# Kernel optimization log

Hardware: AMD Instinct MI355X
Metric: run time of the kernel (lower is better)

## Reference

```python
import jax, jax.numpy as jnp
import numpy as np

U = 100000   # num_users
I = 50000    # num_items
N = U + I    # total nodes
D = 64       # embed_size
L = 3        # n_layers
E = 2000000  # num edges
EPS = 1e-12  # F.normalize default eps


def setup_inputs() -> dict:
    key = jax.random.key(0)
    k1, k2, k3, k4 = jax.random.split(key, 4)
    user_emb = jax.random.normal(k1, (U, D), dtype=jnp.float32) * 0.1
    item_emb = jax.random.normal(k2, (I, D), dtype=jnp.float32) * 0.1
    rows = jax.random.randint(k3, (E,), 0, N, dtype=jnp.int32)
    cols = jax.random.randint(k4, (E,), 0, N, dtype=jnp.int32)
    return {"user_emb": user_emb, "item_emb": item_emb, "rows": rows, "cols": cols}


def _spmm(vals, rows, cols, x):
    # sparse [N,N] @ dense [N,D] via gather + segment reduce
    return jax.ops.segment_sum(vals[:, None] * x[cols], rows, num_segments=N)


def _l2norm(x):
    return x / jnp.maximum(jnp.linalg.norm(x, axis=1, keepdims=True), EPS)


def reference(user_emb, item_emb, rows, cols):
    emb0 = jnp.concatenate([user_emb, item_emb], axis=0)  # [N, D]

    # laplacian_adj: G = D^-1/2 A D^-1/2 on the same edge set
    deg = jax.ops.segment_sum(jnp.ones((E,), emb0.dtype), rows, num_segments=N)
    d_is = jnp.where(deg > 0, deg ** -0.5, 0.0)
    g_vals = d_is[rows] * d_is[cols]  # [E]

    cur = emb0
    acc = emb0
    user_fine, item_fine = [], []
    for _ in range(L):
        gnn = _spmm(g_vals, rows, cols, cur)  # [N, D]
        # fine_laplacian_adj: cosine-sim edge scores, row-normalized
        gr = _l2norm(gnn[rows])
        gc = _l2norm(gnn[cols])
        scores = (jnp.sum(gr * gc, axis=1) + 1.0) * 0.5  # [E] in [0,1]
        rowsum = jax.ops.segment_sum(scores, rows, num_segments=N)
        d_inv = jnp.where(rowsum > 0, 1.0 / rowsum, 0.0)
        fine = _spmm(d_inv[rows] * scores, rows, cols, cur)  # [N, D]
        cur = gnn + fine
        acc = acc + cur
        user_fine.append(fine[:U])
        item_fine.append(fine[U:])

    u_embs = acc[:U]
    i_embs = acc[U:]
    return (u_embs, i_embs, jnp.stack(user_fine, 0), jnp.stack(item_fine, 0))
```

## Files before the change

kernel.cpp:

```cpp
#include <hip/hip_runtime.h>

namespace {

typedef unsigned short u16;
typedef __attribute__((__ext_vector_type__(2))) float f32x2;
typedef __attribute__((__ext_vector_type__(4))) float f32x4;

constexpr int Un = 100000;
constexpr int In = 50000;
constexpr int Nn = 150000;
constexpr int D  = 64;
constexpr int Ln = 3;
constexpr int En = 2000000;
constexpr int CHUNK = 1024;
constexpr int NB = (Nn + CHUNK - 1) / CHUNK;

__device__ __forceinline__ u16 f2bf(float f) {
    unsigned u = __float_as_uint(f);
    unsigned r = (u + 0x7FFFu + ((u >> 16) & 1u)) >> 16;
    return (u16)r;
}
__device__ __forceinline__ float bflo(unsigned u) {
    return __uint_as_float(u << 16);
}
__device__ __forceinline__ float bfhi(unsigned u) {
    return __uint_as_float(u & 0xFFFF0000u);
}
__device__ __forceinline__ unsigned pack2(float lo, float hi) {
    return (unsigned)f2bf(lo) | ((unsigned)f2bf(hi) << 16);
}

__device__ __forceinline__ f32x2 pkfma(f32x2 a, f32x2 b, f32x2 c) {
    f32x2 d;
    asm("v_pk_fma_f32 %0, %1, %2, %3" : "=v"(d) : "v"(a), "v"(b), "v"(c));
    return d;
}
__device__ __forceinline__ f32x2 pkadd(f32x2 a, f32x2 b) {
    f32x2 d;
    asm("v_pk_add_f32 %0, %1, %2" : "=v"(d) : "v"(a), "v"(b));
    return d;
}

__device__ __forceinline__ float dpp_add8(float x) {
    x += __uint_as_float((unsigned)__builtin_amdgcn_update_dpp(
        0, (int)__float_as_uint(x), 0xB1, 0xF, 0xF, true));
    x += __uint_as_float((unsigned)__builtin_amdgcn_update_dpp(
        0, (int)__float_as_uint(x), 0x4E, 0xF, 0xF, true));
    x += __uint_as_float((unsigned)__builtin_amdgcn_update_dpp(
        0, (int)__float_as_uint(x), 0x141, 0xF, 0xF, true));
    return x;
}

__device__ __forceinline__ void unp8(uint4 q, f32x2* o) {
    o[0].x = bflo(q.x); o[0].y = bfhi(q.x);
    o[1].x = bflo(q.y); o[1].y = bfhi(q.y);
    o[2].x = bflo(q.z); o[2].y = bfhi(q.z);
    o[3].x = bflo(q.w); o[3].y = bfhi(q.w);
}

__global__ void count_kernel(const int* __restrict__ rows, int* __restrict__ deg,
                             int* __restrict__ eoff) {
    int e = blockIdx.x * blockDim.x + threadIdx.x;
    if (e < En) eoff[e] = atomicAdd(&deg[rows[e]], 1);
}

__global__ void scan_partial(const int* __restrict__ deg, float* __restrict__ d_is,
                             int* __restrict__ bsum) {
    int tid = threadIdx.x;
    int base = blockIdx.x * CHUNK + tid * 4;
    int s = 0;
#pragma unroll
    for (int i = 0; i < 4; ++i) {
        int idx = base + i;
        if (idx < Nn) {
            int d = deg[idx];
            s += d;
            d_is[idx] = d > 0 ? rsqrtf((float)d) : 0.f;
        }
    }
    __shared__ int sh[256];
    sh[tid] = s;
    __syncthreads();
    for (int o = 128; o > 0; o >>= 1) {
        if (tid < o) sh[tid] += sh[tid + o];
        __syncthreads();
    }
    if (tid == 0) bsum[blockIdx.x] = sh[0];
}

__global__ void scan_top(int* __restrict__ bsum, int* __restrict__ row_ptr) {
    __shared__ int sh[256];
    int tid = threadIdx.x;
    int v = (tid < NB) ? bsum[tid] : 0;
    sh[tid] = v;
    __syncthreads();
    for (int o = 1; o < 256; o <<= 1) {
        int t = (tid >= o) ? sh[tid - o] : 0;
        __syncthreads();
        sh[tid] += t;
        __syncthreads();
    }
    if (tid < NB) bsum[tid] = sh[tid] - v;
    if (tid == 255) row_ptr[Nn] = sh[255];
}

__global__ void scan_final(const int* __restrict__ deg, const int* __restrict__ bsum,
                           int* __restrict__ row_ptr) {
    int tid = threadIdx.x;
    int base = blockIdx.x * CHUNK + tid * 4;
    int v[4];
    int ts = 0;
#pragma unroll
    for (int i = 0; i < 4; ++i) {
        int idx = base + i;
        v[i] = (idx < Nn) ? deg[idx] : 0;
        ts += v[i];
    }
    __shared__ int sh[256];
    sh[tid] = ts;
    __syncthreads();
    for (int o = 1; o < 256; o <<= 1) {
        int t = (tid >= o) ? sh[tid - o] : 0;
        __syncthreads();
        sh[tid] += t;
        __syncthreads();
    }
    int excl = bsum[blockIdx.x] + sh[tid] - ts;
#pragma unroll
    for (int i = 0; i < 4; ++i) {
        int idx = base + i;
        if (idx < Nn) row_ptr[idx] = excl;
        excl += v[i];
    }
}

__global__ void fill_kernel(const int* __restrict__ rows, const int* __restrict__ cols,
                            const int* __restrict__ row_ptr, const int* __restrict__ eoff,
                            int* __restrict__ col_off) {
    int e = blockIdx.x * blockDim.x + threadIdx.x;
    if (e >= En) return;
    col_off[row_ptr[rows[e]] + eoff[e]] = cols[e] << 7;
}

__global__ void init_kernel(const float* __restrict__ ue, const float* __restrict__ ie,
                            const float* __restrict__ d_is,
                            float* __restrict__ out, u16* __restrict__ cur,
                            u16* __restrict__ S) {
    int i = (blockIdx.x * 256 + threadIdx.x) * 4;
    if (i >= Nn * D) return;
    const float* src = (i < Un * D) ? (ue + i) : (ie + (i - Un * D));
    float4 v = *(const float4*)src;
    *(float4*)(out + i) = v;
    ushort4 q;
    q.x = f2bf(v.x); q.y = f2bf(v.y); q.z = f2bf(v.z); q.w = f2bf(v.w);
    *(ushort4*)(cur + i) = q;
    float ds = d_is[i >> 6];
    ushort4 qs;
    qs.x = f2bf(v.x * ds); qs.y = f2bf(v.y * ds);
    qs.z = f2bf(v.z * ds); qs.w = f2bf(v.w * ds);
    *(ushort4*)(S + i) = qs;
}

__global__ __launch_bounds__(256) void spmm_gnn(const u16* __restrict__ S_,
                                                u16* __restrict__ Qn_,
                                                const int* __restrict__ row_ptr,
                                                const int* __restrict__ col_off,
                                                const float* __restrict__ d_is,
                                                float* __restrict__ normv) {
    int r = (blockIdx.x * 256 + threadIdx.x) >> 6;
    if (r >= Nn) return;
    int lane = threadIdx.x & 63;
    int g = lane >> 3, l = lane & 7;
    unsigned l16 = (unsigned)l * 16u;
    const char* pS = (const char*)S_;
    int s = row_ptr[r], t = row_ptr[r + 1];
    float dr = d_is[r];
    f32x2 z; z.x = 0.f; z.y = 0.f;
    f32x2 a2[4] = {z, z, z, z};
    int deg = t - s;
    int nfull = deg >> 3;
    int rem = deg & 7;
    int jb = s + g;
#pragma unroll 2
    for (int i = 0; i < nfull; ++i) {
        unsigned off = (unsigned)col_off[jb + i * 8];
        uint4 q = *(const uint4*)(pS + (off + l16));
        f32x2 x2[4];
        unp8(q, x2);
#pragma unroll
        for (int p = 0; p < 4; ++p) a2[p] = pkadd(a2[p], x2[p]);
    }
    if (g < rem) {
        unsigned off = (unsigned)col_off[jb + nfull * 8];
        uint4 q = *(const uint4*)(pS + (off + l16));
        f32x2 x2[4];
        unp8(q, x2);
#pragma unroll
        for (int p = 0; p < 4; ++p) a2[p] = pkadd(a2[p], x2[p]);
    }
    float a[8] = {a2[0].x, a2[0].y, a2[1].x, a2[1].y,
                  a2[2].x, a2[2].y, a2[3].x, a2[3].y};
#pragma unroll
    for (int k = 0; k < 8; ++k) {
        a[k] += __shfl_xor(a[k], 8);
        a[k] += __shfl_xor(a[k], 16);
        a[k] += __shfl_xor(a[k], 32);
    }
    float sq = 0.f;
#pragma unroll
    for (int k = 0; k < 8; ++k) sq = fmaf(a[k], a[k], sq);
    sq = dpp_add8(sq);
    if (g == 0) {
        float gn = dr * sqrtf(sq);
        float nrm = fmaxf(gn, 1e-12f);
        float scale = dr / nrm;
        normv[r] = nrm;
        unsigned ro = ((unsigned)r << 7) + l16;
        uint4 on;
        on.x = pack2(a[0] * scale, a[1] * scale);
        on.y = pack2(a[2] * scale, a[3] * scale);
        on.z = pack2(a[4] * scale, a[5] * scale);
        on.w = pack2(a[6] * scale, a[7] * scale);
        *(uint4*)((char*)Qn_ + ro) = on;
    }
}

__global__ __launch_bounds__(256) void score_fine_kernel(const u16* __restrict__ A_,
                                                         const u16* __restrict__ Qn_,
                                                         u16* __restrict__ C_,
                                                         u16* __restrict__ S_,
                                                         const float* __restrict__ normv,
                                                         const float* __restrict__ d_is,
                                                         const int* __restrict__ row_ptr,
                                                         const int* __restrict__ col_off,
                                                         float* __restrict__ out, int layer) {
    int r = (blockIdx.x * 256 + threadIdx.x) >> 6;
    if (r >= Nn) return;
    int lane = threadIdx.x & 63;
    int g = lane >> 3, l = lane & 7;
    unsigned l16 = (unsigned)l * 16u;
    const char* pQn = (const char*)Qn_;
    const char* pA  = (const char*)A_;
    int s = row_ptr[r], t = row_ptr[r + 1];
    unsigned ro = ((unsigned)r << 7) + l16;
    uint4 qbn = *(const uint4*)(pQn + ro);
    float nrm = normv[r];
    float dsr = d_is[r];
    f32x2 b2[4];
    unp8(qbn, b2);
    f32x2 z; z.x = 0.f; z.y = 0.f;
    f32x2 facc[4] = {z, z, z, z};
    float rowsum = 0.f;
    int deg = t - s;
    int nfull = deg >> 3;
    int rem = deg & 7;
    int jb = s + g;
#pragma unroll 2
    for (int i = 0; i < nfull; ++i) {
        unsigned off = (unsigned)col_off[jb + i * 8];
        unsigned vo = off + l16;
        uint4 qx = *(const uint4*)(pQn + vo);
        uint4 qy = *(const uint4*)(pA + vo);
        f32x2 x2[4];
        unp8(qx, x2);
        f32x2 d2 = pkfma(b2[0], x2[0], z);
        d2 = pkfma(b2[1], x2[1], d2);
        d2 = pkfma(b2[2], x2[2], d2);
        d2 = pkfma(b2[3], x2[3], d2);
        float d = dpp_add8(d2.x + d2.y);
        float sc = fmaf(d, 0.5f, 0.5f);
        rowsum += sc;
        f32x2 y2[4];
        unp8(qy, y2);
        f32x2 sc2; sc2.x = sc; sc2.y = sc;
#pragma unroll
        for (int p = 0; p < 4; ++p) facc[p] = pkfma(sc2, y2[p], facc[p]);
    }
    if (g < rem) {
        unsigned off = (unsigned)col_off[jb + nfull * 8];
        unsigned vo = off + l16;
        uint4 qx = *(const uint4*)(pQn + vo);
        uint4 qy = *(const uint4*)(pA + vo);
        f32x2 x2[4];
        unp8(qx, x2);
        f32x2 d2 = pkfma(b2[0], x2[0], z);
        d2 = pkfma(b2[1], x2[1], d2);
        d2 = pkfma(b2[2], x2[2], d2);
        d2 = pkfma(b2[3], x2[3], d2);
        float d = dpp_add8(d2.x + d2.y);
        float sc = fmaf(d, 0.5f, 0.5f);
        rowsum += sc;
        f32x2 y2[4];
        unp8(qy, y2);
        f32x2 sc2; sc2.x = sc; sc2.y = sc;
#pragma unroll
        for (int p = 0; p < 4; ++p) facc[p] = pkfma(sc2, y2[p], facc[p]);
    }
    float f[8] = {facc[0].x, facc[0].y, facc[1].x, facc[1].y,
                  facc[2].x, facc[2].y, facc[3].x, facc[3].y};
    rowsum += __shfl_xor(rowsum, 8);
    rowsum += __shfl_xor(rowsum, 16);
    rowsum += __shfl_xor(rowsum, 32);
#pragma unroll
    for (int k = 0; k < 8; ++k) {
        f[k] += __shfl_xor(f[k], 8);
        f[k] += __shfl_xor(f[k], 16);
        f[k] += __shfl_xor(f[k], 32);
    }
    float di = rowsum > 0.f ? 1.f / rowsum : 0.f;
#pragma unroll
    for (int k = 0; k < 8; ++k) f[k] *= di;
    if (g == 0) {
        float bb[8] = {b2[0].x, b2[0].y, b2[1].x, b2[1].y,
                       b2[2].x, b2[2].y, b2[3].x, b2[3].y};
        float cn[8];
#pragma unroll
        for (int k = 0; k < 8; ++k) cn[k] = fmaf(bb[k], nrm, f[k]);
        uint4 qn;
        qn.x = pack2(cn[0], cn[1]); qn.y = pack2(cn[2], cn[3]);
        qn.z = pack2(cn[4], cn[5]); qn.w = pack2(cn[6], cn[7]);
        *(uint4*)((char*)C_ + ro) = qn;
        if (layer != Ln - 1) {
            uint4 qs;
            qs.x = pack2(cn[0] * dsr, cn[1] * dsr);
            qs.y = pack2(cn[2] * dsr, cn[3] * dsr);
            qs.z = pack2(cn[4] * dsr, cn[5] * dsr);
            qs.w = pack2(cn[6] * dsr, cn[7] * dsr);
            *(uint4*)((char*)S_ + ro) = qs;
        }
        float* op = out + (size_t)r * D + l * 8;
        float4 a0 = ((float4*)op)[0], a1 = ((float4*)op)[1];
        a0.x += cn[0]; a0.y += cn[1]; a0.z += cn[2]; a0.w += cn[3];
        a1.x += cn[4]; a1.y += cn[5]; a1.z += cn[6]; a1.w += cn[7];
        ((float4*)op)[0] = a0;
        ((float4*)op)[1] = a1;
        size_t fo;
        if (r < Un)
            fo = (size_t)Nn * D + (size_t)layer * Un * D + (size_t)r * D + l * 8;
        else
            fo = (size_t)Nn * D + (size_t)Ln * Un * D + (size_t)layer * In * D
                 + (size_t)(r - Un) * D + l * 8;
        f32x4 f0, f1;
        f0.x = f[0]; f0.y = f[1]; f0.z = f[2]; f0.w = f[3];
        f1.x = f[4]; f1.y = f[5]; f1.z = f[6]; f1.w = f[7];
        __builtin_nontemporal_store(f0, (f32x4*)(out + fo));
        __builtin_nontemporal_store(f1, (f32x4*)(out + fo) + 1);
    }
}

}

extern "C" void kernel_launch(void* const* d_in, const int* in_sizes, int n_in,
                              void* d_out, int out_size, void* d_ws, size_t ws_size,
                              hipStream_t stream) {
    const float* user_emb = (const float*)d_in[0];
    const float* item_emb = (const float*)d_in[1];
    const int* rows = (const int*)d_in[2];
    const int* cols = (const int*)d_in[3];
    float* out = (float*)d_out;

    char* ws = (char*)d_ws;
    size_t off = 0;
    auto alloc = [&](size_t bytes) -> void* {
        void* p = ws + off;
        off += (bytes + 255) & ~size_t(255);
        return p;
    };
    u16*   buf0    = (u16*)  alloc((size_t)Nn * D * 2);
    u16*   buf1    = (u16*)  alloc((size_t)Nn * D * 2);
    u16*   buf2    = (u16*)  alloc((size_t)Nn * D * 2);
    u16*   buf3    = (u16*)  alloc((size_t)Nn * D * 2);
    int*   col_off = (int*)  alloc((size_t)(En + 8) * 4);
    int*   deg     = (int*)  alloc((size_t)Nn * 4);
    int*   row_ptr = (int*)  alloc((size_t)(Nn + 1) * 4);
    float* d_is    = (float*)alloc((size_t)Nn * 4);
    float* normv   = (float*)alloc((size_t)Nn * 4);
    int*   bsum    = (int*)  alloc(4096);
    int*   eoff    = (int*)buf2;
    (void)ws_size; (void)in_sizes; (void)n_in; (void)out_size;

    hipMemsetAsync(deg, 0, (size_t)Nn * 4, stream);

    const int EB = (En + 255) / 256;
    count_kernel<<<EB, 256, 0, stream>>>(rows, deg, eoff);
    scan_partial<<<NB, 256, 0, stream>>>(deg, d_is, bsum);
    scan_top<<<1, 256, 0, stream>>>(bsum, row_ptr);
    scan_final<<<NB, 256, 0, stream>>>(deg, bsum, row_ptr);
    fill_kernel<<<EB, 256, 0, stream>>>(rows, cols, row_ptr, eoff, col_off);
    init_kernel<<<(Nn * D / 4 + 255) / 256, 256, 0, stream>>>(user_emb, item_emb, d_is,
                                                              out, buf0, buf3);

    const int RB = Nn / 4;
    u16* P = buf0;
    u16* R = buf1;
    u16* Qn = buf2;
    u16* S  = buf3;
    for (int l = 0; l < Ln; ++l) {
        spmm_gnn<<<RB, 256, 0, stream>>>(S, Qn, row_ptr, col_off, d_is, normv);
        score_fine_kernel<<<RB, 256, 0, stream>>>(P, Qn, R, S, normv, d_is,
                                                  row_ptr, col_off, out, l);
        u16* tmp = P; P = R; R = tmp;
    }
}
```

Measured before the change: 788.2 us.

## Map one row per 8-lane group with degree-sorted row ordering

```diff
diff --git a/kernel.cpp b/kernel.cpp
--- a/kernel.cpp
+++ b/kernel.cpp
@@ -14,6 +14,8 @@
 constexpr int En = 2000000;
 constexpr int CHUNK = 1024;
 constexpr int NB = (Nn + CHUNK - 1) / CHUNK;
+constexpr int DCAP = 128;
+constexpr int NW = Nn / 8;
 
 __device__ __forceinline__ u16 f2bf(float f) {
     unsigned u = __float_as_uint(f);
@@ -140,6 +142,49 @@
     int e = blockIdx.x * blockDim.x + threadIdx.x;
     if (e >= En) return;
     col_off[row_ptr[rows[e]] + eoff[e]] = cols[e] << 7;
+}
+
+__global__ void hist_kernel(const int* __restrict__ deg, int* __restrict__ hist) {
+    __shared__ int lh[DCAP];
+    int tid = threadIdx.x;
+    if (tid < DCAP) lh[tid] = 0;
+    __syncthreads();
+    int i = blockIdx.x * 256 + tid;
+    if (i < Nn) atomicAdd(&lh[min(deg[i], DCAP - 1)], 1);
+    __syncthreads();
+    if (tid < DCAP) {
+        int v = lh[tid];
+        if (v) atomicAdd(&hist[tid], v);
+    }
+}
+
+__global__ void hist_scan(int* __restrict__ hist) {
+    __shared__ int sh[DCAP];
+    int tid = threadIdx.x;
+    int v = hist[tid];
+    sh[tid] = v;
+    __syncthreads();
+    for (int o = 1; o < DCAP; o <<= 1) {
+        int t = (tid >= o) ? sh[tid - o] : 0;
+        __syncthreads();
+        sh[tid] += t;
+        __syncthreads();
+    }
+    hist[tid] = sh[tid] - v;
+}
+
+__global__ void perm_kernel(const int* __restrict__ deg, const int* __restrict__ row_ptr,
+                            const float* __restrict__ d_is, int* __restrict__ hist,
+                            int4* __restrict__ srt) {
+    int i = blockIdx.x * 256 + threadIdx.x;
+    if (i >= Nn) return;
+    int p = atomicAdd(&hist[min(deg[i], DCAP - 1)], 1);
+    int4 v;
+    v.x = row_ptr[i];
+    v.y = row_ptr[i + 1];
+    v.z = __float_as_int(d_is[i]);
+    v.w = i;
+    srt[p] = v;
 }
 
 __global__ void init_kernel(const float* __restrict__ ue, const float* __restrict__ ie,
@@ -163,101 +208,82 @@
 
 __global__ __launch_bounds__(256) void spmm_gnn(const u16* __restrict__ S_,
                                                 u16* __restrict__ Qn_,
-                                                const int* __restrict__ row_ptr,
+                                                const int4* __restrict__ srt,
                                                 const int* __restrict__ col_off,
-                                                const float* __restrict__ d_is,
-                                                float* __restrict__ normv) {
-    int r = (blockIdx.x * 256 + threadIdx.x) >> 6;
-    if (r >= Nn) return;
+                                                float* __restrict__ normv_s) {
+    int w = (blockIdx.x * 256 + threadIdx.x) >> 6;
+    if (w >= NW) return;
     int lane = threadIdx.x & 63;
     int g = lane >> 3, l = lane & 7;
     unsigned l16 = (unsigned)l * 16u;
+    int wb = w * 8 + g;
+    int4 q4 = srt[wb];
+    int s = q4.x, t = q4.y;
+    float dr = __int_as_float(q4.z);
+    int r = q4.w;
     const char* pS = (const char*)S_;
-    int s = row_ptr[r], t = row_ptr[r + 1];
-    float dr = d_is[r];
     f32x2 z; z.x = 0.f; z.y = 0.f;
     f32x2 a2[4] = {z, z, z, z};
-    int deg = t - s;
-    int nfull = deg >> 3;
-    int rem = deg & 7;
-    int jb = s + g;
 #pragma unroll 2
-    for (int i = 0; i < nfull; ++i) {
-        unsigned off = (unsigned)col_off[jb + i * 8];
+    for (int j = s; j < t; ++j) {
+        unsigned off = (unsigned)col_off[j];
         uint4 q = *(const uint4*)(pS + (off + l16));
         f32x2 x2[4];
         unp8(q, x2);
 #pragma unroll
         for (int p = 0; p < 4; ++p) a2[p] = pkadd(a2[p], x2[p]);
     }
-    if (g < rem) {
-        unsigned off = (unsigned)col_off[jb + nfull * 8];
-        uint4 q = *(const uint4*)(pS + (off + l16));
-        f32x2 x2[4];
-        unp8(q, x2);
-#pragma unroll
-        for (int p = 0; p < 4; ++p) a2[p] = pkadd(a2[p], x2[p]);
-    }
-    float a[8] = {a2[0].x, a2[0].y, a2[1].x, a2[1].y,
-                  a2[2].x, a2[2].y, a2[3].x, a2[3].y};
-#pragma unroll
-    for (int k = 0; k < 8; ++k) {
-        a[k] += __shfl_xor(a[k], 8);
-        a[k] += __shfl_xor(a[k], 16);
-        a[k] += __shfl_xor(a[k], 32);
-    }
     float sq = 0.f;
 #pragma unroll
-    for (int k = 0; k < 8; ++k) sq = fmaf(a[k], a[k], sq);
+    for (int p = 0; p < 4; ++p) {
+        sq = fmaf(a2[p].x, a2[p].x, sq);
+        sq = fmaf(a2[p].y, a2[p].y, sq);
+    }
     sq = dpp_add8(sq);
-    if (g == 0) {
-        float gn = dr * sqrtf(sq);
-        float nrm = fmaxf(gn, 1e-12f);
-        float scale = dr / nrm;
-        normv[r] = nrm;
-        unsigned ro = ((unsigned)r << 7) + l16;
-        uint4 on;
-        on.x = pack2(a[0] * scale, a[1] * scale);
-        on.y = pack2(a[2] * scale, a[3] * scale);
-        on.z = pack2(a[4] * scale, a[5] * scale);
-        on.w = pack2(a[6] * scale, a[7] * scale);
-        *(uint4*)((char*)Qn_ + ro) = on;
-    }
+    float gn = dr * sqrtf(sq);
+    float nrm = fmaxf(gn, 1e-12f);
+    float scale = dr / nrm;
+    if (l == 0) normv_s[wb] = nrm;
+    unsigned ro = ((unsigned)r << 7) + l16;
+    uint4 on;
+    on.x = pack2(a2[0].x * scale, a2[0].y * scale);
+    on.y = pack2(a2[1].x * scale, a2[1].y * scale);
+    on.z = pack2(a2[2].x * scale, a2[2].y * scale);
+    on.w = pack2(a2[3].x * scale, a2[3].y * scale);
+    *(uint4*)((char*)Qn_ + ro) = on;
 }
 
 __global__ __launch_bounds__(256) void score_fine_kernel(const u16* __restrict__ A_,
                                                          const u16* __restrict__ Qn_,
                                                          u16* __restrict__ C_,
                                                          u16* __restrict__ S_,
-                                                         const float* __restrict__ normv,
-                                                         const float* __restrict__ d_is,
-                                                         const int* __restrict__ row_ptr,
+                                                         const float* __restrict__ normv_s,
+                                                         const int4* __restrict__ srt,
                                                          const int* __restrict__ col_off,
                                                          float* __restrict__ out, int layer) {
-    int r = (blockIdx.x * 256 + threadIdx.x) >> 6;
-    if (r >= Nn) return;
+    int w = (blockIdx.x * 256 + threadIdx.x) >> 6;
+    if (w >= NW) return;
     int lane = threadIdx.x & 63;
     int g = lane >> 3, l = lane & 7;
     unsigned l16 = (unsigned)l * 16u;
+    int wb = w * 8 + g;
+    int4 q4 = srt[wb];
+    int s = q4.x, t = q4.y;
+    float dsr = __int_as_float(q4.z);
+    int r = q4.w;
+    float nrm = normv_s[wb];
     const char* pQn = (const char*)Qn_;
     const char* pA  = (const char*)A_;
-    int s = row_ptr[r], t = row_ptr[r + 1];
     unsigned ro = ((unsigned)r << 7) + l16;
     uint4 qbn = *(const uint4*)(pQn + ro);
-    float nrm = normv[r];
-    float dsr = d_is[r];
     f32x2 b2[4];
     unp8(qbn, b2);
     f32x2 z; z.x = 0.f; z.y = 0.f;
     f32x2 facc[4] = {z, z, z, z};
     float rowsum = 0.f;
-    int deg = t - s;
-    int nfull = deg >> 3;
-    int rem = deg & 7;
-    int jb = s + g;
 #pragma unroll 2
-    for (int i = 0; i < nfull; ++i) {
-        unsigned off = (unsigned)col_off[jb + i * 8];
+    for (int j = s; j < t; ++j) {
+        unsigned off = (unsigned)col_off[j];
         unsigned vo = off + l16;
         uint4 qx = *(const uint4*)(pQn + vo);
         uint4 qy = *(const uint4*)(pA + vo);
@@ -276,76 +302,43 @@
 #pragma unroll
         for (int p = 0; p < 4; ++p) facc[p] = pkfma(sc2, y2[p], facc[p]);
     }
-    if (g < rem) {
-        unsigned off = (unsigned)col_off[jb + nfull * 8];
-        unsigned vo = off + l16;
-        uint4 qx = *(const uint4*)(pQn + vo);
-        uint4 qy = *(const uint4*)(pA + vo);
-        f32x2 x2[4];
-        unp8(qx, x2);
-        f32x2 d2 = pkfma(b2[0], x2[0], z);
-        d2 = pkfma(b2[1], x2[1], d2);
-        d2 = pkfma(b2[2], x2[2], d2);
-        d2 = pkfma(b2[3], x2[3], d2);
-        float d = dpp_add8(d2.x + d2.y);
-        float sc = fmaf(d, 0.5f, 0.5f);
-        rowsum += sc;
-        f32x2 y2[4];
-        unp8(qy, y2);
-        f32x2 sc2; sc2.x = sc; sc2.y = sc;
-#pragma unroll
-        for (int p = 0; p < 4; ++p) facc[p] = pkfma(sc2, y2[p], facc[p]);
-    }
-    float f[8] = {facc[0].x, facc[0].y, facc[1].x, facc[1].y,
-                  facc[2].x, facc[2].y, facc[3].x, facc[3].y};
-    rowsum += __shfl_xor(rowsum, 8);
-    rowsum += __shfl_xor(rowsum, 16);
-    rowsum += __shfl_xor(rowsum, 32);
-#pragma unroll
-    for (int k = 0; k < 8; ++k) {
-        f[k] += __shfl_xor(f[k], 8);
-        f[k] += __shfl_xor(f[k], 16);
-        f[k] += __shfl_xor(f[k], 32);
-    }
     float di = rowsum > 0.f ? 1.f / rowsum : 0.f;
-#pragma unroll
-    for (int k = 0; k < 8; ++k) f[k] *= di;
-    if (g == 0) {
-        float bb[8] = {b2[0].x, b2[0].y, b2[1].x, b2[1].y,
-                       b2[2].x, b2[2].y, b2[3].x, b2[3].y};
-        float cn[8];
-#pragma unroll
-        for (int k = 0; k < 8; ++k) cn[k] = fmaf(bb[k], nrm, f[k]);
-        uint4 qn;
-        qn.x = pack2(cn[0], cn[1]); qn.y = pack2(cn[2], cn[3]);
-        qn.z = pack2(cn[4], cn[5]); qn.w = pack2(cn[6], cn[7]);
-        *(uint4*)((char*)C_ + ro) = qn;
-        if (layer != Ln - 1) {
-            uint4 qs;
-            qs.x = pack2(cn[0] * dsr, cn[1] * dsr);
-            qs.y = pack2(cn[2] * dsr, cn[3] * dsr);
-            qs.z = pack2(cn[4] * dsr, cn[5] * dsr);
-            qs.w = pack2(cn[6] * dsr, cn[7] * dsr);
-            *(uint4*)((char*)S_ + ro) = qs;
-        }
-        float* op = out + (size_t)r * D + l * 8;
-        float4 a0 = ((float4*)op)[0], a1 = ((float4*)op)[1];
-        a0.x += cn[0]; a0.y += cn[1]; a0.z += cn[2]; a0.w += cn[3];
-        a1.x += cn[4]; a1.y += cn[5]; a1.z += cn[6]; a1.w += cn[7];
-        ((float4*)op)[0] = a0;
-        ((float4*)op)[1] = a1;
-        size_t fo;
-        if (r < Un)
-            fo = (size_t)Nn * D + (size_t)layer * Un * D + (size_t)r * D + l * 8;
-        else
-            fo = (size_t)Nn * D + (size_t)Ln * Un * D + (size_t)layer * In * D
-                 + (size_t)(r - Un) * D + l * 8;
-        f32x4 f0, f1;
-        f0.x = f[0]; f0.y = f[1]; f0.z = f[2]; f0.w = f[3];
-        f1.x = f[4]; f1.y = f[5]; f1.z = f[6]; f1.w = f[7];
-        __builtin_nontemporal_store(f0, (f32x4*)(out + fo));
-        __builtin_nontemporal_store(f1, (f32x4*)(out + fo) + 1);
-    }
+    float f[8] = {facc[0].x * di, facc[0].y * di, facc[1].x * di, facc[1].y * di,
+                  facc[2].x * di, facc[2].y * di, facc[3].x * di, facc[3].y * di};
+    float bb[8] = {b2[0].x, b2[0].y, b2[1].x, b2[1].y,
+                   b2[2].x, b2[2].y, b2[3].x, b2[3].y};
+    float cn[8];
+#pragma unroll
+    for (int k = 0; k < 8; ++k) cn[k] = fmaf(bb[k], nrm, f[k]);
+    uint4 qn;
+    qn.x = pack2(cn[0], cn[1]); qn.y = pack2(cn[2], cn[3]);
+    qn.z = pack2(cn[4], cn[5]); qn.w = pack2(cn[6], cn[7]);
+    *(uint4*)((char*)C_ + ro) = qn;
+    if (layer != Ln - 1) {
+        uint4 qs;
+        qs.x = pack2(cn[0] * dsr, cn[1] * dsr);
+        qs.y = pack2(cn[2] * dsr, cn[3] * dsr);
+        qs.z = pack2(cn[4] * dsr, cn[5] * dsr);
+        qs.w = pack2(cn[6] * dsr, cn[7] * dsr);
+        *(uint4*)((char*)S_ + ro) = qs;
+    }
+    float* op = out + (size_t)r * D + l * 8;
+    float4 a0 = ((float4*)op)[0], a1 = ((float4*)op)[1];
+    a0.x += cn[0]; a0.y += cn[1]; a0.z += cn[2]; a0.w += cn[3];
+    a1.x += cn[4]; a1.y += cn[5]; a1.z += cn[6]; a1.w += cn[7];
+    ((float4*)op)[0] = a0;
+    ((float4*)op)[1] = a1;
+    size_t fo;
+    if (r < Un)
+        fo = (size_t)Nn * D + (size_t)layer * Un * D + (size_t)r * D + l * 8;
+    else
+        fo = (size_t)Nn * D + (size_t)Ln * Un * D + (size_t)layer * In * D
+             + (size_t)(r - Un) * D + l * 8;
+    f32x4 f0, f1;
+    f0.x = f[0]; f0.y = f[1]; f0.z = f[2]; f0.w = f[3];
+    f1.x = f[4]; f1.y = f[5]; f1.z = f[6]; f1.w = f[7];
+    __builtin_nontemporal_store(f0, (f32x4*)(out + fo));
+    __builtin_nontemporal_store(f1, (f32x4*)(out + fo) + 1);
 }
 
 }
@@ -374,31 +367,38 @@
     int*   deg     = (int*)  alloc((size_t)Nn * 4);
     int*   row_ptr = (int*)  alloc((size_t)(Nn + 1) * 4);
     float* d_is    = (float*)alloc((size_t)Nn * 4);
-    float* normv   = (float*)alloc((size_t)Nn * 4);
+    float* normv_s = (float*)alloc((size_t)Nn * 4);
+    int4*  srt     = (int4*) alloc((size_t)Nn * 16);
+    int*   hist    = (int*)  alloc(DCAP * 4);
     int*   bsum    = (int*)  alloc(4096);
     int*   eoff    = (int*)buf2;
     (void)ws_size; (void)in_sizes; (void)n_in; (void)out_size;
 
     hipMemsetAsync(deg, 0, (size_t)Nn * 4, stream);
+    hipMemsetAsync(hist, 0, DCAP * 4, stream);
 
     const int EB = (En + 255) / 256;
+    const int RB256 = (Nn + 255) / 256;
     count_kernel<<<EB, 256, 0, stream>>>(rows, deg, eoff);
+    hist_kernel<<<RB256, 256, 0, stream>>>(deg, hist);
     scan_partial<<<NB, 256, 0, stream>>>(deg, d_is, bsum);
     scan_top<<<1, 256, 0, stream>>>(bsum, row_ptr);
     scan_final<<<NB, 256, 0, stream>>>(deg, bsum, row_ptr);
+    hist_scan<<<1, DCAP, 0, stream>>>(hist);
     fill_kernel<<<EB, 256, 0, stream>>>(rows, cols, row_ptr, eoff, col_off);
+    perm_kernel<<<RB256, 256, 0, stream>>>(deg, row_ptr, d_is, hist, srt);
     init_kernel<<<(Nn * D / 4 + 255) / 256, 256, 0, stream>>>(user_emb, item_emb, d_is,
                                                               out, buf0, buf3);
 
-    const int RB = Nn / 4;
+    const int WB = (NW * 64 + 255) / 256;
     u16* P = buf0;
     u16* R = buf1;
     u16* Qn = buf2;
     u16* S  = buf3;
     for (int l = 0; l < Ln; ++l) {
-        spmm_gnn<<<RB, 256, 0, stream>>>(S, Qn, row_ptr, col_off, d_is, normv);
-        score_fine_kernel<<<RB, 256, 0, stream>>>(P, Qn, R, S, normv, d_is,
-                                                  row_ptr, col_off, out, l);
+        spmm_gnn<<<WB, 256, 0, stream>>>(S, Qn, srt, col_off, normv_s);
+        score_fine_kernel<<<WB, 256, 0, stream>>>(P, Qn, R, S, normv_s, srt,
+                                                  col_off, out, l);
         u16* tmp = P; P = R; R = tmp;
     }
 }
```

Result: slower. 1.238 ms (+57.1%).

## Defer fp32 accumulation to a final pass and spread degree atomics and stores

Applied to the files above, without the earlier changes.

```diff
diff --git a/kernel.cpp b/kernel.cpp
--- a/kernel.cpp
+++ b/kernel.cpp
@@ -14,6 +14,7 @@
 constexpr int En = 2000000;
 constexpr int CHUNK = 1024;
 constexpr int NB = (Nn + CHUNK - 1) / CHUNK;
+constexpr int DSTR = 8;
 
 __device__ __forceinline__ u16 f2bf(float f) {
     unsigned u = __float_as_uint(f);
@@ -58,13 +59,13 @@
     o[3].x = bflo(q.w); o[3].y = bfhi(q.w);
 }
 
-__global__ void count_kernel(const int* __restrict__ rows, int* __restrict__ deg,
+__global__ void count_kernel(const int* __restrict__ rows, int* __restrict__ deg8,
                              int* __restrict__ eoff) {
     int e = blockIdx.x * blockDim.x + threadIdx.x;
-    if (e < En) eoff[e] = atomicAdd(&deg[rows[e]], 1);
-}
-
-__global__ void scan_partial(const int* __restrict__ deg, float* __restrict__ d_is,
+    if (e < En) eoff[e] = atomicAdd(&deg8[(size_t)rows[e] * DSTR], 1);
+}
+
+__global__ void scan_partial(const int* __restrict__ deg8, float* __restrict__ d_is,
                              int* __restrict__ bsum) {
     int tid = threadIdx.x;
     int base = blockIdx.x * CHUNK + tid * 4;
@@ -73,7 +74,7 @@
     for (int i = 0; i < 4; ++i) {
         int idx = base + i;
         if (idx < Nn) {
-            int d = deg[idx];
+            int d = deg8[(size_t)idx * DSTR];
             s += d;
             d_is[idx] = d > 0 ? rsqrtf((float)d) : 0.f;
         }
@@ -104,7 +105,7 @@
     if (tid == 255) row_ptr[Nn] = sh[255];
 }
 
-__global__ void scan_final(const int* __restrict__ deg, const int* __restrict__ bsum,
+__global__ void scan_final(const int* __restrict__ deg8, const int* __restrict__ bsum,
                            int* __restrict__ row_ptr) {
     int tid = threadIdx.x;
     int base = blockIdx.x * CHUNK + tid * 4;
@@ -113,7 +114,7 @@
 #pragma unroll
     for (int i = 0; i < 4; ++i) {
         int idx = base + i;
-        v[i] = (idx < Nn) ? deg[idx] : 0;
+        v[i] = (idx < Nn) ? deg8[(size_t)idx * DSTR] : 0;
         ts += v[i];
     }
     __shared__ int sh[256];
@@ -144,21 +145,21 @@
 
 __global__ void init_kernel(const float* __restrict__ ue, const float* __restrict__ ie,
                             const float* __restrict__ d_is,
-                            float* __restrict__ out, u16* __restrict__ cur,
-                            u16* __restrict__ S) {
-    int i = (blockIdx.x * 256 + threadIdx.x) * 4;
-    if (i >= Nn * D) return;
-    const float* src = (i < Un * D) ? (ue + i) : (ie + (i - Un * D));
-    float4 v = *(const float4*)src;
-    *(float4*)(out + i) = v;
-    ushort4 q;
-    q.x = f2bf(v.x); q.y = f2bf(v.y); q.z = f2bf(v.z); q.w = f2bf(v.w);
-    *(ushort4*)(cur + i) = q;
-    float ds = d_is[i >> 6];
-    ushort4 qs;
-    qs.x = f2bf(v.x * ds); qs.y = f2bf(v.y * ds);
-    qs.z = f2bf(v.z * ds); qs.w = f2bf(v.w * ds);
-    *(ushort4*)(S + i) = qs;
+                            u16* __restrict__ cur, u16* __restrict__ S) {
+    int i8 = (blockIdx.x * 256 + threadIdx.x) * 8;
+    if (i8 >= Nn * D) return;
+    const float* src = (i8 < Un * D) ? (ue + i8) : (ie + (i8 - Un * D));
+    float4 v0 = ((const float4*)src)[0];
+    float4 v1 = ((const float4*)src)[1];
+    uint4 qc;
+    qc.x = pack2(v0.x, v0.y); qc.y = pack2(v0.z, v0.w);
+    qc.z = pack2(v1.x, v1.y); qc.w = pack2(v1.z, v1.w);
+    *(uint4*)((char*)cur + (size_t)i8 * 2) = qc;
+    float ds = d_is[i8 >> 6];
+    uint4 qs;
+    qs.x = pack2(v0.x * ds, v0.y * ds); qs.y = pack2(v0.z * ds, v0.w * ds);
+    qs.z = pack2(v1.x * ds, v1.y * ds); qs.w = pack2(v1.z * ds, v1.w * ds);
+    *(uint4*)((char*)S + (size_t)i8 * 2) = qs;
 }
 
 __global__ __launch_bounds__(256) void spmm_gnn(const u16* __restrict__ S_,
@@ -210,11 +211,11 @@
 #pragma unroll
     for (int k = 0; k < 8; ++k) sq = fmaf(a[k], a[k], sq);
     sq = dpp_add8(sq);
+    float gn = dr * sqrtf(sq);
+    float nrm = fmaxf(gn, 1e-12f);
+    float scale = dr / nrm;
+    if (lane == 8) normv[r] = nrm;
     if (g == 0) {
-        float gn = dr * sqrtf(sq);
-        float nrm = fmaxf(gn, 1e-12f);
-        float scale = dr / nrm;
-        normv[r] = nrm;
         unsigned ro = ((unsigned)r << 7) + l16;
         uint4 on;
         on.x = pack2(a[0] * scale, a[1] * scale);
@@ -242,10 +243,10 @@
     const char* pQn = (const char*)Qn_;
     const char* pA  = (const char*)A_;
     int s = row_ptr[r], t = row_ptr[r + 1];
+    float dsr = d_is[r];
+    float nrm = normv[r];
     unsigned ro = ((unsigned)r << 7) + l16;
     uint4 qbn = *(const uint4*)(pQn + ro);
-    float nrm = normv[r];
-    float dsr = d_is[r];
     f32x2 b2[4];
     unp8(qbn, b2);
     f32x2 z; z.x = 0.f; z.y = 0.f;
@@ -310,42 +311,66 @@
     float di = rowsum > 0.f ? 1.f / rowsum : 0.f;
 #pragma unroll
     for (int k = 0; k < 8; ++k) f[k] *= di;
+    float bb[8] = {b2[0].x, b2[0].y, b2[1].x, b2[1].y,
+                   b2[2].x, b2[2].y, b2[3].x, b2[3].y};
+    float cn[8];
+#pragma unroll
+    for (int k = 0; k < 8; ++k) cn[k] = fmaf(bb[k], nrm, f[k]);
     if (g == 0) {
-        float bb[8] = {b2[0].x, b2[0].y, b2[1].x, b2[1].y,
-                       b2[2].x, b2[2].y, b2[3].x, b2[3].y};
-        float cn[8];
-#pragma unroll
-        for (int k = 0; k < 8; ++k) cn[k] = fmaf(bb[k], nrm, f[k]);
         uint4 qn;
         qn.x = pack2(cn[0], cn[1]); qn.y = pack2(cn[2], cn[3]);
         qn.z = pack2(cn[4], cn[5]); qn.w = pack2(cn[6], cn[7]);
         *(uint4*)((char*)C_ + ro) = qn;
-        if (layer != Ln - 1) {
-            uint4 qs;
-            qs.x = pack2(cn[0] * dsr, cn[1] * dsr);
-            qs.y = pack2(cn[2] * dsr, cn[3] * dsr);
-            qs.z = pack2(cn[4] * dsr, cn[5] * dsr);
-            qs.w = pack2(cn[6] * dsr, cn[7] * dsr);
-            *(uint4*)((char*)S_ + ro) = qs;
-        }
-        float* op = out + (size_t)r * D + l * 8;
-        float4 a0 = ((float4*)op)[0], a1 = ((float4*)op)[1];
-        a0.x += cn[0]; a0.y += cn[1]; a0.z += cn[2]; a0.w += cn[3];
-        a1.x += cn[4]; a1.y += cn[5]; a1.z += cn[6]; a1.w += cn[7];
-        ((float4*)op)[0] = a0;
-        ((float4*)op)[1] = a1;
+    }
+    if (g == 1 && layer != Ln - 1) {
+        uint4 qs;
+        qs.x = pack2(cn[0] * dsr, cn[1] * dsr);
+        qs.y = pack2(cn[2] * dsr, cn[3] * dsr);
+        qs.z = pack2(cn[4] * dsr, cn[5] * dsr);
+        qs.w = pack2(cn[6] * dsr, cn[7] * dsr);
+        *(uint4*)((char*)S_ + ro) = qs;
+    }
+    if (g >= 2 && g <= 3) {
         size_t fo;
         if (r < Un)
             fo = (size_t)Nn * D + (size_t)layer * Un * D + (size_t)r * D + l * 8;
         else
             fo = (size_t)Nn * D + (size_t)Ln * Un * D + (size_t)layer * In * D
                  + (size_t)(r - Un) * D + l * 8;
-        f32x4 f0, f1;
-        f0.x = f[0]; f0.y = f[1]; f0.z = f[2]; f0.w = f[3];
-        f1.x = f[4]; f1.y = f[5]; f1.z = f[6]; f1.w = f[7];
-        __builtin_nontemporal_store(f0, (f32x4*)(out + fo));
-        __builtin_nontemporal_store(f1, (f32x4*)(out + fo) + 1);
-    }
+        if (g == 2) {
+            f32x4 f0; f0.x = f[0]; f0.y = f[1]; f0.z = f[2]; f0.w = f[3];
+            __builtin_nontemporal_store(f0, (f32x4*)(out + fo));
+        } else {
+            f32x4 f1; f1.x = f[4]; f1.y = f[5]; f1.z = f[6]; f1.w = f[7];
+            __builtin_nontemporal_store(f1, (f32x4*)(out + fo) + 1);
+        }
+    }
+}
+
+__global__ void final_sum(const float* __restrict__ ue, const float* __restrict__ ie,
+                          const u16* __restrict__ c1, const u16* __restrict__ c2,
+                          const u16* __restrict__ c3, float* __restrict__ out) {
+    int i8 = (blockIdx.x * 256 + threadIdx.x) * 8;
+    if (i8 >= Nn * D) return;
+    const float* src = (i8 < Un * D) ? (ue + i8) : (ie + (i8 - Un * D));
+    float4 v0 = ((const float4*)src)[0];
+    float4 v1 = ((const float4*)src)[1];
+    uint4 q1 = *(const uint4*)((const char*)c1 + (size_t)i8 * 2);
+    uint4 q2 = *(const uint4*)((const char*)c2 + (size_t)i8 * 2);
+    uint4 q3 = *(const uint4*)((const char*)c3 + (size_t)i8 * 2);
+    float o[8] = {v0.x, v0.y, v0.z, v0.w, v1.x, v1.y, v1.z, v1.w};
+    f32x2 t1[4], t2[4], t3[4];
+    unp8(q1, t1); unp8(q2, t2); unp8(q3, t3);
+#pragma unroll
+    for (int p = 0; p < 4; ++p) {
+        o[2 * p]     = ((o[2 * p]     + t1[p].x) + t2[p].x) + t3[p].x;
+        o[2 * p + 1] = ((o[2 * p + 1] + t1[p].y) + t2[p].y) + t3[p].y;
+    }
+    float4 w0, w1;
+    w0.x = o[0]; w0.y = o[1]; w0.z = o[2]; w0.w = o[3];
+    w1.x = o[4]; w1.y = o[5]; w1.z = o[6]; w1.w = o[7];
+    ((float4*)(out + i8))[0] = w0;
+    ((float4*)(out + i8))[1] = w1;
 }
 
 }
@@ -366,39 +391,38 @@
         off += (bytes + 255) & ~size_t(255);
         return p;
     };
-    u16*   buf0    = (u16*)  alloc((size_t)Nn * D * 2);
-    u16*   buf1    = (u16*)  alloc((size_t)Nn * D * 2);
-    u16*   buf2    = (u16*)  alloc((size_t)Nn * D * 2);
-    u16*   buf3    = (u16*)  alloc((size_t)Nn * D * 2);
+    u16*   bufA    = (u16*)  alloc((size_t)Nn * D * 2);
+    u16*   bufB    = (u16*)  alloc((size_t)Nn * D * 2);
+    u16*   bufC    = (u16*)  alloc((size_t)Nn * D * 2);
+    u16*   Qn      = (u16*)  alloc((size_t)Nn * D * 2);
+    u16*   S       = (u16*)  alloc((size_t)Nn * D * 2);
     int*   col_off = (int*)  alloc((size_t)(En + 8) * 4);
-    int*   deg     = (int*)  alloc((size_t)Nn * 4);
+    int*   deg8    = (int*)  alloc((size_t)Nn * DSTR * 4);
     int*   row_ptr = (int*)  alloc((size_t)(Nn + 1) * 4);
     float* d_is    = (float*)alloc((size_t)Nn * 4);
     float* normv   = (float*)alloc((size_t)Nn * 4);
     int*   bsum    = (int*)  alloc(4096);
-    int*   eoff    = (int*)buf2;
+    int*   eoff    = (int*)Qn;
     (void)ws_size; (void)in_sizes; (void)n_in; (void)out_size;
 
-    hipMemsetAsync(deg, 0, (size_t)Nn * 4, stream);
+    hipMemsetAsync(deg8, 0, (size_t)Nn * DSTR * 4, stream);
 
     const int EB = (En + 255) / 256;
-    count_kernel<<<EB, 256, 0, stream>>>(rows, deg, eoff);
-    scan_partial<<<NB, 256, 0, stream>>>(deg, d_is, bsum);
+    count_kernel<<<EB, 256, 0, stream>>>(rows, deg8, eoff);
+    scan_partial<<<NB, 256, 0, stream>>>(deg8, d_is, bsum);
     scan_top<<<1, 256, 0, stream>>>(bsum, row_ptr);
-    scan_final<<<NB, 256, 0, stream>>>(deg, bsum, row_ptr);
+    scan_final<<<NB, 256, 0, stream>>>(deg8, bsum, row_ptr);
     fill_kernel<<<EB, 256, 0, stream>>>(rows, cols, row_ptr, eoff, col_off);
-    init_kernel<<<(Nn * D / 4 + 255) / 256, 256, 0, stream>>>(user_emb, item_emb, d_is,
-                                                              out, buf0, buf3);
+    init_kernel<<<(Nn * D / 8 + 255) / 256, 256, 0, stream>>>(user_emb, item_emb, d_is,
+                                                              bufA, S);
 
     const int RB = Nn / 4;
-    u16* P = buf0;
-    u16* R = buf1;
-    u16* Qn = buf2;
-    u16* S  = buf3;
+    u16* Pl[4] = {bufA, bufB, bufC, bufA};
     for (int l = 0; l < Ln; ++l) {
         spmm_gnn<<<RB, 256, 0, stream>>>(S, Qn, row_ptr, col_off, d_is, normv);
-        score_fine_kernel<<<RB, 256, 0, stream>>>(P, Qn, R, S, normv, d_is,
-                                                  row_ptr, col_off, out, l);
-        u16* tmp = P; P = R; R = tmp;
-    }
-}
+        score_fine_kernel<<<RB, 256, 0, stream>>>(Pl[l], Qn, Pl[l + 1], S, normv,
+                                                  d_is, row_ptr, col_off, out, l);
+    }
+    final_sum<<<(Nn * D / 8 + 255) / 256, 256, 0, stream>>>(user_emb, item_emb,
+                                                            bufB, bufC, bufA, out);
+}
```

After: 764.5 us (median of 2 runs). 3.0% less time.
